# Optimization experiments

Measured on AMD Instinct MI355X. Metric: run time of the kernel, lower is better.

## Reference

```python
import jax, jax.numpy as jnp
import numpy as np

IMG = 32
CX = CY = IMG // 2
B = 65536


def setup_inputs() -> dict:
    key = jax.random.key(0)
    k1, k2, k3 = jax.random.split(key, 3)
    W = jax.random.normal(k1, (B, 16), dtype=jnp.float32)
    noise_randn = jax.random.normal(k2, (B, IMG, IMG), dtype=jnp.float32)
    noise_rand = jax.random.uniform(k3, (B, IMG, IMG), dtype=jnp.float32)
    return {"W": W, "noise_randn": noise_randn, "noise_rand": noise_rand}


def reference(W, noise_randn, noise_rand):
    H = IMG
    PI = jnp.float32(np.pi)
    ar = jnp.arange(H, dtype=jnp.float32)
    xx, yy = jnp.meshgrid(ar, ar, indexing="ij")  # (H, H)

    def c(k):  # per-sample scalar broadcast to (B,1,1)
        return W[:, k][:, None, None]

    r = jnp.sqrt((xx - CX) ** 2 + (yy - CY) ** 2)  # (H, H)

    # layer 0: clipped radial cone
    img = jnp.clip(c(0) * 5 - r, 0.0, 1.0)
    # layer 1: centered square (torch int(clamp(...).item()) == floor for positive vals)
    half = jnp.floor(jnp.clip(jnp.abs(c(1)) * 8, 2.0, 12.0))
    mask1 = ((xx >= CY - half) & (xx < CY + half) & (yy >= CX - half) & (yy < CX + half))
    img = img + 0.5 * mask1.astype(jnp.float32)
    # layers 2-4: sinusoids
    img = img + 0.5 * jnp.sin(c(2) * 10 * PI * xx / H)
    img = img + 0.5 * jnp.sin(c(3) * 10 * PI * yy / H)
    img = img + 0.5 * jnp.sin(c(4) * 5 * PI * (xx + yy) / (2 * H))
    # layer 5: warp
    img = img + 0.5 * jnp.sin((yy + c(5) * 10) * PI / H)
    # layer 6: bias
    img = img + c(6)
    # layer 7: gaussian blob; int() truncates toward zero
    bx = jnp.trunc(CX + c(7) * 5)
    by = jnp.trunc(CY + c(7) * 5)
    sigma = 4.0 + jnp.abs(c(7)) * 4.0
    img = img + jnp.exp(-((xx - bx) ** 2 + (yy - by) ** 2) / (2 * sigma ** 2))
    # layer 8: ring
    img = img + ((r - c(8) * 10) ** 2 < 10.0).astype(jnp.float32)
    # layer 9: checkerboard; cb_size = int(clamp(|w|*8+2, 2, 16)) -> floor
    cb = jnp.floor(jnp.clip(jnp.abs(c(9)) * 8 + 2, 2.0, 16.0))
    img = img + jnp.mod(jnp.floor(xx / cb) + jnp.floor(yy / cb), 2.0) * 0.3
    # layer 10: rotated line
    angle = c(10) * PI
    rot_line = jnp.cos(angle) * (xx - CX) + jnp.sin(angle) * (yy - CY)
    img = img + (jnp.abs(rot_line) < 3.0).astype(jnp.float32) * 0.6
    # layer 11: angular sinusoid
    theta = jnp.arctan2(yy - CY, xx - CX)
    img = img + 0.5 * jnp.sin(theta * c(11) * 5)
    # layers 12-13: noise (deterministic inputs replace randn_like/rand_like)
    img = img + noise_randn * 0.1 * c(12)
    img = img + (noise_rand - 0.5) * c(13) * 0.05
    # layer 14: contrast
    img = (img - 0.5) * (1.0 + c(14)) + 0.5
    # layer 15: conditional inversion
    img = jnp.where(c(15) > 0, 1.0 - img, img)
    # per-image min-max normalize
    mn = jnp.min(img, axis=(1, 2), keepdims=True)
    mx = jnp.max(img, axis=(1, 2), keepdims=True)
    img = (img - mn) / (mx - mn + 1e-8)
    return img[:, None, :, :]  # (B, 1, H, W)
```

## Files before the change

### kernel.cpp

```cpp
#include <hip/hip_runtime.h>
#include <math.h>

#define NB 65536
#define IMGD 32
#define NPIX 1024
#define PSTRIDE 20

__device__ float g_r[NPIX];
__device__ float g_th[NPIX];
__device__ float g_par[(size_t)NB * PSTRIDE];

__global__ void init_tables_kernel() {
    int p = threadIdx.x;
    int x = p >> 5, y = p & 31;
    float dx = (float)(x - 16), dy = (float)(y - 16);
    g_r[p] = sqrtf(dx * dx + dy * dy);
    g_th[p] = atan2f(dy, dx) * 0.79577471545947668f;
}

__global__ void init_params_kernel(const float* __restrict__ W) {
    int b = blockIdx.x * blockDim.x + threadIdx.x;
    if (b >= NB) return;
    const float* w = W + (size_t)b * 16;
    float* P = g_par + (size_t)b * PSTRIDE;

    float w0 = w[0], w1 = w[1], w2 = w[2], w3 = w[3], w4 = w[4], w5 = w[5],
          w6 = w[6], w7 = w[7], w8 = w[8], w9 = w[9], w10 = w[10], w11 = w[11],
          w12 = w[12], w13 = w[13], w14 = w[14], w15 = w[15];

    P[0] = w0 * 5.0f;
    float half = floorf(fminf(fmaxf(fabsf(w1) * 8.0f, 2.0f), 12.0f));
    P[1] = 16.0f - half;
    P[2] = 16.0f + half;
    P[3] = w2 * 0.15625f;
    P[4] = w3 * 0.15625f;
    P[5] = w4 * 0.0390625f;
    P[6] = w5 * 0.15625f;
    P[7] = w6;
    float t7 = __fadd_rn(16.0f, __fmul_rn(w7, 5.0f));
    P[8] = truncf(t7);
    float sg = 4.0f + fabsf(w7) * 4.0f;
    P[9] = -1.0f / (2.0f * sg * sg);
    P[10] = w8 * 10.0f;
    float cb = floorf(fminf(fmaxf(__fadd_rn(fabsf(w9) * 8.0f, 2.0f), 2.0f), 16.0f));
    P[11] = cb;
    P[12] = 1.0f / cb;
    float ang = __fmul_rn(w10, 3.14159265358979323846f);
    P[13] = (float)cos((double)ang);
    P[14] = (float)sin((double)ang);
    P[15] = w11;
    P[16] = w12 * 0.1f;
    P[17] = w13 * 0.05f;
    P[18] = 1.0f + w14;
    P[19] = w15;
}

__device__ __forceinline__ float hsin(float rev) {
    rev = rev - floorf(rev);
    return __builtin_amdgcn_sinf(rev);
}

__device__ __forceinline__ float fdivq(float xf, float cb, float rcb) {
    float q = floorf(xf * rcb);
    q += ((q + 1.0f) * cb <= xf) ? 1.0f : 0.0f;
    q -= ((q * cb) > xf) ? 1.0f : 0.0f;
    return q;
}

__global__ __launch_bounds__(256) void decode_kernel(
        const float* __restrict__ nrand,
        const float* __restrict__ nunif,
        float* __restrict__ out) {
    int b = blockIdx.x;
    int t = threadIdx.x;
    const float* P = g_par + (size_t)b * PSTRIDE;

    float a0  = P[0],  lo  = P[1],  hi  = P[2],  s2  = P[3],  s3 = P[4];
    float s4  = P[5],  s5o = P[6],  w6  = P[7],  bxy = P[8],  nk = P[9];
    float t8  = P[10], cb  = P[11], rcb = P[12], ca  = P[13], sa = P[14];
    float w11 = P[15], k12 = P[16], k13 = P[17], con = P[18], w15 = P[19];

    __shared__ float4 xt4[32];
    __shared__ float4 yt4[32];
    __shared__ float  stab[63];

    if (t < 32) {
        float xf = (float)t;
        float qx = fdivq(xf, cb, rcb);
        float px = qx - 2.0f * floorf(qx * 0.5f);
        float d  = xf - bxy;
        float4 e;
        e.x = 0.5f * hsin(s2 * xf) + 0.3f * px;
        e.y = (xf >= lo && xf < hi) ? 1.0f : 0.0f;
        e.z = -0.6f * px;
        e.w = __expf(d * d * nk);
        xt4[t] = e;
    } else if (t < 64) {
        float yf = (float)(t - 32);
        float qy = fdivq(yf, cb, rcb);
        float py = qy - 2.0f * floorf(qy * 0.5f);
        float d  = yf - bxy;
        float4 e;
        e.x = 0.5f * hsin(s3 * yf) + 0.5f * hsin(0.015625f * yf + s5o)
              + 0.3f * py + w6;
        e.y = (yf >= lo && yf < hi) ? 0.5f : 0.0f;
        e.z = py;
        e.w = __expf(d * d * nk);
        yt4[t - 32] = e;
    } else if (t < 127) {
        int s = t - 64;
        stab[s] = 0.5f * hsin(s4 * (float)s);
    }
    __syncthreads();

    int p0 = t * 4;
    int x  = p0 >> 5;
    int y0 = p0 & 31;
    float xf = (float)x;

    float4 X   = xt4[x];
    float rotx = __fmul_rn(ca, xf - 16.0f);

    size_t base = (size_t)b * NPIX + (size_t)p0;
    float4 vr = *reinterpret_cast<const float4*>(nrand + base);
    float4 vu = *reinterpret_cast<const float4*>(nunif + base);
    float4 rr = *reinterpret_cast<const float4*>(g_r + p0);
    float4 tt = *reinterpret_cast<const float4*>(g_th + p0);

    const float* rrp = reinterpret_cast<const float*>(&rr);
    const float* ttp = reinterpret_cast<const float*>(&tt);
    const float* vrp = reinterpret_cast<const float*>(&vr);
    const float* vup = reinterpret_cast<const float*>(&vu);

    float img[4];
    float mn = 1e30f, mx = -1e30f;

#pragma unroll
    for (int j = 0; j < 4; ++j) {
        int   y  = y0 + j;
        float yf = (float)y;
        float r  = rrp[j];
        float4 Y = yt4[y];

        float v = fminf(fmaxf(a0 - r, 0.0f), 1.0f);
        v += X.x + Y.x;
        v = fmaf(X.y, Y.y, v);
        v += stab[x + y];
        v = fmaf(X.z, Y.z, v);
        v = fmaf(X.w, Y.w, v);
        float dr = __fsub_rn(r, t8);
        v += (__fmul_rn(dr, dr) < 10.0f) ? 1.0f : 0.0f;
        float rot = __fadd_rn(rotx, __fmul_rn(sa, yf - 16.0f));
        v += (fabsf(rot) < 3.0f) ? 0.6f : 0.0f;
        v += 0.5f * hsin(ttp[j] * w11);
        v = fmaf(vrp[j], k12, v);
        v = fmaf(vup[j] - 0.5f, k13, v);

        img[j] = v;
        mn = fminf(mn, v);
        mx = fmaxf(mx, v);
    }

#pragma unroll
    for (int off = 32; off > 0; off >>= 1) {
        mn = fminf(mn, __shfl_xor(mn, off));
        mx = fmaxf(mx, __shfl_xor(mx, off));
    }
    __shared__ float smn[4], smx[4];
    int wid = t >> 6;
    if ((t & 63) == 0) { smn[wid] = mn; smx[wid] = mx; }
    __syncthreads();
    mn = fminf(fminf(smn[0], smn[1]), fminf(smn[2], smn[3]));
    mx = fmaxf(fmaxf(smx[0], smx[1]), fmaxf(smx[2], smx[3]));

    float ac    = fabsf(con);
    float denom = fmaf(ac, mx - mn, 1e-8f);
    float s     = ac / denom;
    bool  eff   = (w15 > 0.0f) != (con < 0.0f);
    float bse   = eff ? mx : mn;
    float sgn   = eff ? -s : s;

    float4 o;
    o.x = (img[0] - bse) * sgn;
    o.y = (img[1] - bse) * sgn;
    o.z = (img[2] - bse) * sgn;
    o.w = (img[3] - bse) * sgn;
    *reinterpret_cast<float4*>(out + base) = o;
}

extern "C" void kernel_launch(void* const* d_in, const int* in_sizes, int n_in,
                              void* d_out, int out_size, void* d_ws, size_t ws_size,
                              hipStream_t stream) {
    const float* W  = (const float*)d_in[0];
    const float* nr = (const float*)d_in[1];
    const float* nu = (const float*)d_in[2];
    float* out = (float*)d_out;

    init_tables_kernel<<<1, 1024, 0, stream>>>();
    init_params_kernel<<<NB / 256, 256, 0, stream>>>(W);
    decode_kernel<<<NB, 256, 0, stream>>>(nr, nu, out);
}
```

Baseline: 148.7 us.

## Remap pixels to row-strided scalar access and fold table init into params kernel

The decode kernel now gives each thread one column y and four rows strided by 8. Global loads and stores become scalar but still coalesced across the wave, in place of float4 per thread. The per-column Y entry is loaded once per thread and the per-row X entry is read per iteration, with padding on the yt4 shared array to avoid bank conflicts. The r/theta table initialisation moves into block 0 of the params kernel, which removes one launch. The cost is more load instructions in exchange for less shared-memory traffic and one fewer kernel launch.

```diff
diff --git a/kernel.cpp b/kernel.cpp
--- a/kernel.cpp
+++ b/kernel.cpp
@@ -10,16 +10,19 @@
 __device__ float g_th[NPIX];
 __device__ float g_par[(size_t)NB * PSTRIDE];
 
-__global__ void init_tables_kernel() {
-    int p = threadIdx.x;
-    int x = p >> 5, y = p & 31;
-    float dx = (float)(x - 16), dy = (float)(y - 16);
-    g_r[p] = sqrtf(dx * dx + dy * dy);
-    g_th[p] = atan2f(dy, dx) * 0.79577471545947668f;
-}
-
 __global__ void init_params_kernel(const float* __restrict__ W) {
     int b = blockIdx.x * blockDim.x + threadIdx.x;
+
+    if (blockIdx.x == 0) {
+        int t = threadIdx.x;
+        for (int k = 0; k < 4; ++k) {
+            int p = t * 4 + k;
+            int x = p >> 5, y = p & 31;
+            float dx = (float)(x - 16), dy = (float)(y - 16);
+            g_r[p] = sqrtf(dx * dx + dy * dy);
+            g_th[p] = atan2f(dy, dx) * 0.79577471545947668f;
+        }
+    }
     if (b >= NB) return;
     const float* w = W + (size_t)b * 16;
     float* P = g_par + (size_t)b * PSTRIDE;
@@ -81,7 +84,7 @@
     float w11 = P[15], k12 = P[16], k13 = P[17], con = P[18], w15 = P[19];
 
     __shared__ float4 xt4[32];
-    __shared__ float4 yt4[32];
+    __shared__ float4 yt4[36];
     __shared__ float  stab[63];
 
     if (t < 32) {
@@ -96,7 +99,8 @@
         e.w = __expf(d * d * nk);
         xt4[t] = e;
     } else if (t < 64) {
-        float yf = (float)(t - 32);
+        int   y  = t - 32;
+        float yf = (float)y;
         float qy = fdivq(yf, cb, rcb);
         float py = qy - 2.0f * floorf(qy * 0.5f);
         float d  = yf - bxy;
@@ -106,41 +110,34 @@
         e.y = (yf >= lo && yf < hi) ? 0.5f : 0.0f;
         e.z = py;
         e.w = __expf(d * d * nk);
-        yt4[t - 32] = e;
+        yt4[y + (y >> 3)] = e;
     } else if (t < 127) {
         int s = t - 64;
         stab[s] = 0.5f * hsin(s4 * (float)s);
     }
     __syncthreads();
 
-    int p0 = t * 4;
-    int x  = p0 >> 5;
-    int y0 = p0 & 31;
-    float xf = (float)x;
+    int   y   = t & 31;
+    int   x0  = t >> 5;
+    float4 Y  = yt4[y + (y >> 3)];
+    float yf  = (float)y;
+    float sy  = __fmul_rn(sa, yf - 16.0f);
 
-    float4 X   = xt4[x];
-    float rotx = __fmul_rn(ca, xf - 16.0f);
-
-    size_t base = (size_t)b * NPIX + (size_t)p0;
-    float4 vr = *reinterpret_cast<const float4*>(nrand + base);
-    float4 vu = *reinterpret_cast<const float4*>(nunif + base);
-    float4 rr = *reinterpret_cast<const float4*>(g_r + p0);
-    float4 tt = *reinterpret_cast<const float4*>(g_th + p0);
-
-    const float* rrp = reinterpret_cast<const float*>(&rr);
-    const float* ttp = reinterpret_cast<const float*>(&tt);
-    const float* vrp = reinterpret_cast<const float*>(&vr);
-    const float* vup = reinterpret_cast<const float*>(&vu);
+    size_t base = (size_t)b * NPIX + (size_t)t;
+    const float* nrp = nrand + base;
+    const float* nup = nunif + base;
+    const float* rp  = g_r + t;
+    const float* tp  = g_th + t;
 
     float img[4];
     float mn = 1e30f, mx = -1e30f;
 
 #pragma unroll
     for (int j = 0; j < 4; ++j) {
-        int   y  = y0 + j;
-        float yf = (float)y;
-        float r  = rrp[j];
-        float4 Y = yt4[y];
+        int   x  = x0 + 8 * j;
+        float xf = (float)x;
+        float r  = rp[256 * j];
+        float4 X = xt4[x];
 
         float v = fminf(fmaxf(a0 - r, 0.0f), 1.0f);
         v += X.x + Y.x;
@@ -150,11 +147,11 @@
         v = fmaf(X.w, Y.w, v);
         float dr = __fsub_rn(r, t8);
         v += (__fmul_rn(dr, dr) < 10.0f) ? 1.0f : 0.0f;
-        float rot = __fadd_rn(rotx, __fmul_rn(sa, yf - 16.0f));
+        float rot = __fadd_rn(__fmul_rn(ca, xf - 16.0f), sy);
         v += (fabsf(rot) < 3.0f) ? 0.6f : 0.0f;
-        v += 0.5f * hsin(ttp[j] * w11);
-        v = fmaf(vrp[j], k12, v);
-        v = fmaf(vup[j] - 0.5f, k13, v);
+        v += 0.5f * hsin(tp[256 * j] * w11);
+        v = fmaf(nrp[256 * j], k12, v);
+        v = fmaf(nup[256 * j] - 0.5f, k13, v);
 
         img[j] = v;
         mn = fminf(mn, v);
@@ -180,12 +177,10 @@
     float bse   = eff ? mx : mn;
     float sgn   = eff ? -s : s;
 
-    float4 o;
-    o.x = (img[0] - bse) * sgn;
-    o.y = (img[1] - bse) * sgn;
-    o.z = (img[2] - bse) * sgn;
-    o.w = (img[3] - bse) * sgn;
-    *reinterpret_cast<float4*>(out + base) = o;
+    float* op = out + base;
+#pragma unroll
+    for (int j = 0; j < 4; ++j)
+        op[256 * j] = (img[j] - bse) * sgn;
 }
 
 extern "C" void kernel_launch(void* const* d_in, const int* in_sizes, int n_in,
@@ -196,7 +191,6 @@
     const float* nu = (const float*)d_in[2];
     float* out = (float*)d_out;
 
-    init_tables_kernel<<<1, 1024, 0, stream>>>();
     init_params_kernel<<<NB / 256, 256, 0, stream>>>(W);
     decode_kernel<<<NB, 256, 0, stream>>>(nr, nu, out);
 }
```

Result: no change. 147.2 us (-1.0%).
